# Optimization experiments

Hardware: AMD Instinct MI355X
Metric: run time of the kernel (lower is better)

Reference implementation:

```python
import jax, jax.numpy as jnp
import numpy as np

N = 100000   # nodes
E = 1600000  # edges
D = 128      # input feature dim
H = 128      # hidden dim
L = 3        # gnn layers
G = 64       # graphs in batch
C = 2        # classes


def setup_inputs() -> dict:
    key = jax.random.key(0)
    ks = jax.random.split(key, 12)
    s = 0.05
    x = jax.random.normal(ks[0], (N, D), jnp.float32)
    edge_index = jax.random.randint(ks[1], (2, E), 0, N, dtype=jnp.int32)
    batch = jnp.sort(jax.random.randint(ks[2], (N,), 0, G, dtype=jnp.int32))
    return {
        "x": x,
        "edge_index": edge_index,
        "batch": batch,
        "W0": jax.random.normal(ks[3], (D, H), jnp.float32) * s,
        "b0": jnp.zeros((H,), jnp.float32),
        "Wg": jax.random.normal(ks[4], (L, H, H), jnp.float32) * s,
        "bg": jnp.zeros((L, H), jnp.float32),
        "Wc1": jax.random.normal(ks[5], (H, H), jnp.float32) * s,
        "bc1": jnp.zeros((H,), jnp.float32),
        "Wc2": jax.random.normal(ks[6], (H, C), jnp.float32) * s,
        "bc2": jnp.zeros((C,), jnp.float32),
    }


def reference(x, edge_index, batch, W0, b0, Wg, bg, Wc1, bc1, Wc2, bc2):
    # --- GCN normalization with self-loops (PyG gcn_norm) ---
    src, dst = edge_index[0], edge_index[1]
    loops = jnp.arange(N, dtype=src.dtype)
    src_f = jnp.concatenate([src, loops])  # [E+N] message sources (x_j)
    dst_f = jnp.concatenate([dst, loops])  # [E+N] aggregation targets
    deg = jax.ops.segment_sum(jnp.ones((E + N,), x.dtype), dst_f, num_segments=N)
    dinv = jnp.where(deg > 0, jax.lax.rsqrt(deg), 0.0)
    norm = (dinv[src_f] * dinv[dst_f])[:, None]  # [E+N, 1]

    # --- input linear + relu (dropout is identity in eval mode) ---
    h = jax.nn.relu(x @ W0 + b0)  # [N, H]

    # --- stacked GCNConv layers with residual + relu ---
    for l in range(L):
        xw = h @ Wg[l]  # [N, H]
        agg = jax.ops.segment_sum(xw[src_f] * norm, dst_f, num_segments=N) + bg[l]
        h = jax.nn.relu(h + agg)

    # --- global add pool over graphs ---
    pooled = jax.ops.segment_sum(h, batch, num_segments=G)  # [G, H]

    # --- classifier MLP + softmax ---
    z = jax.nn.relu(pooled @ Wc1 + bc1)
    return jax.nn.softmax(z @ Wc2 + bc2, axis=-1)  # [G, C]
```

## Files before the change

### kernel.cpp

```cpp
#include <hip/hip_runtime.h>

#define NN 100000
#define NE 1600000
#define HD 128
#define NG 64
#define NL 3
#define NBK 391
#define NEB 391
#define CAP 4608
#define NRB 6250
#define FP4_SCALE 8.0f
#define FP4_INV   0.125f

typedef __attribute__((ext_vector_type(8))) short bf16x8;
typedef __attribute__((ext_vector_type(4))) float f32x4;
typedef __attribute__((ext_vector_type(2))) float f32x2;
union U4 { uint4 u; bf16x8 b; };


__device__ __forceinline__ unsigned f2bf(float f) {
    unsigned u = __float_as_uint(f);
    return (u + 0x7FFFu + ((u >> 16) & 1u)) >> 16;
}
__device__ __forceinline__ float bf_lo(unsigned w) { return __uint_as_float(w << 16); }
__device__ __forceinline__ float bf_hi(unsigned w) { return __uint_as_float(w & 0xFFFF0000u); }
__device__ __forceinline__ unsigned cvt_pk_bf16(float lo, float hi) {
    unsigned r;
    asm("v_cvt_pk_bf16_f32 %0, %1, %2" : "=v"(r) : "v"(lo), "v"(hi));
    return r;
}


__global__ __launch_bounds__(256) void k_pre(const float* __restrict__ W0,
                                             const float* __restrict__ Wg,
                                             unsigned* __restrict__ Wb,
                                             const int* __restrict__ src,
                                             const int* __restrict__ dst,
                                             int* __restrict__ gcur,
                                             unsigned* __restrict__ pairs,
                                             const int* __restrict__ batch,
                                             int* __restrict__ start) {
    int blk = blockIdx.x;
    if (blk < 32) {
        int gid = blk * 256 + threadIdx.x;
        for (int i = gid; i < 4 * 8192; i += 32 * 256) {
            int m = i >> 13;
            int r = i & 8191;
            int col = r & 127;
            int p = r >> 7;
            int k0, k1;
            if (m == 0) { k0 = 2 * p; k1 = 2 * p + 1; }
            else        { k0 = p;     k1 = p + 64;    }
            const float* Ws = (m == 0) ? W0 : (Wg + (m - 1) * 16384);
            float w0 = Ws[k0 * 128 + col];
            float w1 = Ws[k1 * 128 + col];
            Wb[m * 8192 + col * 64 + (((2 * p) ^ ((col & 7) << 3)) >> 1)] = (f2bf(w1) << 16) | f2bf(w0);
        }
    } else if (blk < 32 + NEB) {
        __shared__ int cnt[NBK];
        __shared__ int bse[NBK];
        __shared__ int rnk[NBK];
        for (int i = threadIdx.x; i < NBK; i += 256) { cnt[i] = 0; rnk[i] = 0; }
        __syncthreads();
        int base = (blk - 32) * 4096;
        int d[16];
#pragma unroll
        for (int j = 0; j < 16; j++) {
            int e = base + j * 256 + threadIdx.x;
            d[j] = (e < NE) ? dst[e] : -1;
            if (d[j] >= 0) atomicAdd(&cnt[((unsigned)d[j]) >> 8], 1);
        }
        __syncthreads();
        for (int i = threadIdx.x; i < NBK; i += 256) {
            int c = cnt[i];
            bse[i] = c ? atomicAdd(&gcur[i], c) : 0;
        }
        __syncthreads();
#pragma unroll
        for (int j = 0; j < 16; j++) {
            int e = base + j * 256 + threadIdx.x;
            if (e < NE) {
                int b = ((unsigned)d[j]) >> 8;
                int r = atomicAdd(&rnk[b], 1);
                int pos = bse[b] + r;
                if (pos < CAP)
                    pairs[(size_t)b * CAP + pos] = (unsigned)src[e] | (((unsigned)d[j] & 255u) << 17);
            }
        }
    } else {
        int i = (blk - 32 - NEB) * 256 + threadIdx.x;
        if (i >= NN) return;
        int b = batch[i];
        int prev = (i == 0) ? -1 : batch[i - 1];
        for (int g = prev + 1; g <= b; g++) start[g] = i;
        if (i == NN - 1) {
            for (int g = b + 1; g <= NG; g++) start[g] = NN;
        }
    }
}


__global__ __launch_bounds__(256) void k_bfill(const unsigned* __restrict__ pairs,
                                               const int* __restrict__ gcur,
                                               int* __restrict__ row_ptr, int* __restrict__ degA,
                                               float* __restrict__ dinv, unsigned* __restrict__ csr) {
    __shared__ int cnt[256];
    __shared__ int cur[256];
    __shared__ int wsum[4];
    int t = threadIdx.x, k = blockIdx.x;
    int base = k * CAP;
    int ne = min(gcur[k], CAP);
    cnt[t] = 0;
    __syncthreads();
    for (int e = t; e < ne; e += 256) atomicAdd(&cnt[pairs[base + e] >> 17], 1);
    __syncthreads();
    int v = cnt[t];
    int lane = t & 63, wv = t >> 6;
    int sc = v;
#pragma unroll
    for (int off = 1; off < 64; off <<= 1) {
        int n = __shfl_up(sc, off);
        if (lane >= off) sc += n;
    }
    if (lane == 63) wsum[wv] = sc;
    __syncthreads();
    int wbase = 0;
#pragma unroll
    for (int wi = 0; wi < 3; wi++) if (wi < wv) wbase += wsum[wi];
    int excl = base + wbase + sc - v;
    int node = (k << 8) + t;
    if (node < NN) {
        row_ptr[node] = excl;
        degA[node] = v;
        dinv[node] = rsqrtf((float)(v + 1));
    }
    cur[t] = excl;
    __syncthreads();
    for (int e = t; e < ne; e += 256) {
        unsigned p = pairs[base + e];
        int pos = atomicAdd(&cur[p >> 17], 1);
        csr[pos] = (p & 0x1FFFFu) << 6;
    }
}


template <int MODE>
__global__ __launch_bounds__(256) void k_mgemm(
    const float* __restrict__ Xf, const unsigned* __restrict__ Xb,
    const unsigned* __restrict__ Wb, const float* __restrict__ bias,
    const float* __restrict__ dinv, unsigned* __restrict__ Out) {
    __shared__ unsigned short Bt[128 * 128];
    {
        const uint4* s4 = (const uint4*)Wb;
        uint4* d4 = (uint4*)Bt;
        for (int i = threadIdx.x; i < 2048; i += 256) d4[i] = s4[i];
    }
    __syncthreads();

    int lane = threadIdx.x & 63;
    int l15 = lane & 15, q = lane >> 4;
    int rb = blockIdx.x * 4 + (threadIdx.x >> 6);
    if (rb >= NRB) return;
    int r0 = rb * 16;

    U4 a[4];
    if (MODE == 0) {
        const float* xrow = Xf + (size_t)(r0 + l15) * 128 + q * 8;
#pragma unroll
        for (int kk = 0; kk < 4; kk++) {
            float4 f0 = *(const float4*)(xrow + kk * 32);
            float4 f1 = *(const float4*)(xrow + kk * 32 + 4);
            a[kk].u.x = (f2bf(f0.y) << 16) | f2bf(f0.x);
            a[kk].u.y = (f2bf(f0.w) << 16) | f2bf(f0.z);
            a[kk].u.z = (f2bf(f1.y) << 16) | f2bf(f1.x);
            a[kk].u.w = (f2bf(f1.w) << 16) | f2bf(f1.z);
        }
    } else {
        const unsigned* xrow = Xb + (size_t)(r0 + l15) * 64 + q * 4;
#pragma unroll
        for (int kk = 0; kk < 4; kk++) a[kk].u = *(const uint4*)(xrow + kk * 16);
    }

    f32x4 acc[8];
#pragma unroll
    for (int ct = 0; ct < 8; ct++) acc[ct] = (f32x4){0.f, 0.f, 0.f, 0.f};
#pragma unroll
    for (int kk = 0; kk < 4; kk++) {
#pragma unroll
        for (int ct = 0; ct < 8; ct++) {
            int col = ct * 16 + l15;
            int off = col * 128 + ((kk * 32 + q * 8) ^ ((col & 7) << 3));
            U4 b;
            b.u = *(const uint4*)&Bt[off];
            acc[ct] = __builtin_amdgcn_mfma_f32_16x16x32_bf16(a[kk].b, b.b, acc[ct], 0, 0, 0);
        }
    }

    if (MODE == 0) {
        float bv[8];
#pragma unroll
        for (int ct = 0; ct < 8; ct++) bv[ct] = bias[ct * 16 + l15];
#pragma unroll
        for (int r = 0; r < 4; r++) {
            int row = r0 + q * 4 + r;
#pragma unroll
            for (int ct = 0; ct < 4; ct++) {
                float lo = fmaxf(acc[ct][r] + bv[ct], 0.f);
                float hi = fmaxf(acc[ct + 4][r] + bv[ct + 4], 0.f);
                Out[(size_t)row * 64 + ct * 16 + l15] = cvt_pk_bf16(lo, hi);
            }
        }
    } else {
#pragma unroll
        for (int r = 0; r < 4; r++) {
            int row = r0 + q * 4 + r;
            float sc = dinv[row] * FP4_SCALE;
            unsigned dw = __builtin_amdgcn_cvt_scalef32_pk_fp4_f32(0u, acc[0][r] * sc, acc[4][r] * sc, 1.0f, 0);
            dw = __builtin_amdgcn_cvt_scalef32_pk_fp4_f32(dw, acc[2][r] * sc, acc[6][r] * sc, 1.0f, 1);
            dw = __builtin_amdgcn_cvt_scalef32_pk_fp4_f32(dw, acc[1][r] * sc, acc[5][r] * sc, 1.0f, 2);
            dw = __builtin_amdgcn_cvt_scalef32_pk_fp4_f32(dw, acc[3][r] * sc, acc[7][r] * sc, 1.0f, 3);
            Out[(size_t)row * 16 + l15] = dw;
        }
    }
}


__global__ __launch_bounds__(256) void k_aggregate(const unsigned char* __restrict__ xb,
                                                   unsigned* __restrict__ hb,
                                                   const int* __restrict__ row_ptr,
                                                   const int* __restrict__ degA,
                                                   const unsigned* __restrict__ csr,
                                                   const float* __restrict__ dinv,
                                                   const float* __restrict__ bg) {
    int wave = threadIdx.x >> 6;
    int lane = threadIdx.x & 63;
    int q = lane >> 4;
    int l16 = lane & 15;
    int sub = l16 >> 3;
    int l8 = l16 & 7;
    int node = blockIdx.x * 16 + wave * 4 + q;
    unsigned e = (unsigned)row_ptr[node];
    unsigned e1 = e + (unsigned)degA[node];
    unsigned loff = (unsigned)l8 * 8u;

    f32x2 p0 = {0.f, 0.f}, p1 = {0.f, 0.f}, p2 = {0.f, 0.f}, p3 = {0.f, 0.f};
    f32x2 q0 = {0.f, 0.f}, q1 = {0.f, 0.f}, q2 = {0.f, 0.f}, q3 = {0.f, 0.f};

#define ACC8(V) \
    p0 += __builtin_amdgcn_cvt_scalef32_pk_f32_fp4((V).x, 1.0f, 0); \
    p1 += __builtin_amdgcn_cvt_scalef32_pk_f32_fp4((V).x, 1.0f, 1); \
    p2 += __builtin_amdgcn_cvt_scalef32_pk_f32_fp4((V).x, 1.0f, 2); \
    p3 += __builtin_amdgcn_cvt_scalef32_pk_f32_fp4((V).x, 1.0f, 3); \
    q0 += __builtin_amdgcn_cvt_scalef32_pk_f32_fp4((V).y, 1.0f, 0); \
    q1 += __builtin_amdgcn_cvt_scalef32_pk_f32_fp4((V).y, 1.0f, 1); \
    q2 += __builtin_amdgcn_cvt_scalef32_pk_f32_fp4((V).y, 1.0f, 2); \
    q3 += __builtin_amdgcn_cvt_scalef32_pk_f32_fp4((V).y, 1.0f, 3);

    for (; e + 7 < e1; e += 8) {
        unsigned o0 = csr[e + sub];
        unsigned o1 = csr[e + 2 + sub];
        unsigned o2 = csr[e + 4 + sub];
        unsigned o3 = csr[e + 6 + sub];
        uint2 v0 = *(const uint2*)(xb + (o0 + loff));
        uint2 v1 = *(const uint2*)(xb + (o1 + loff));
        uint2 v2 = *(const uint2*)(xb + (o2 + loff));
        uint2 v3 = *(const uint2*)(xb + (o3 + loff));
        ACC8(v0); ACC8(v1); ACC8(v2); ACC8(v3);
    }
    if (e + 3 < e1) {
        unsigned o0 = csr[e + sub];
        unsigned o1 = csr[e + 2 + sub];
        uint2 v0 = *(const uint2*)(xb + (o0 + loff));
        uint2 v1 = *(const uint2*)(xb + (o1 + loff));
        ACC8(v0); ACC8(v1);
        e += 4;
    }
    if (e + 1 < e1) {
        unsigned o = csr[e + sub];
        uint2 v = *(const uint2*)(xb + (o + loff));
        ACC8(v);
        e += 2;
    }
    if (e + (unsigned)sub < e1) {
        unsigned o = csr[e + sub];
        uint2 v = *(const uint2*)(xb + (o + loff));
        ACC8(v);
    }
#undef ACC8

    f32x2 s0 = sub ? q0 : p0;
    f32x2 s1 = sub ? q1 : p1;
    f32x2 s2 = sub ? q2 : p2;
    f32x2 s3 = sub ? q3 : p3;
    f32x2 t0 = sub ? p0 : q0;
    f32x2 t1 = sub ? p1 : q1;
    f32x2 t2 = sub ? p2 : q2;
    f32x2 t3 = sub ? p3 : q3;
    s0.x += __shfl_xor(t0.x, 8); s0.y += __shfl_xor(t0.y, 8);
    s1.x += __shfl_xor(t1.x, 8); s1.y += __shfl_xor(t1.y, 8);
    s2.x += __shfl_xor(t2.x, 8); s2.y += __shfl_xor(t2.y, 8);
    s3.x += __shfl_xor(t3.x, 8); s3.y += __shfl_xor(t3.y, 8);

    int j_e = 2 * l8 + sub;

    unsigned ovd = *(const unsigned*)(xb + (((unsigned)node << 6) + (unsigned)j_e * 4u));
    s0 += __builtin_amdgcn_cvt_scalef32_pk_f32_fp4(ovd, 1.0f, 0);
    s1 += __builtin_amdgcn_cvt_scalef32_pk_f32_fp4(ovd, 1.0f, 1);
    s2 += __builtin_amdgcn_cvt_scalef32_pk_f32_fp4(ovd, 1.0f, 2);
    s3 += __builtin_amdgcn_cvt_scalef32_pk_f32_fp4(ovd, 1.0f, 3);

    float di2 = dinv[node] * FP4_INV;
    float a[8] = {s0.x, s0.y, s1.x, s1.y, s2.x, s2.y, s3.x, s3.y};
    size_t hbase = (size_t)node * 64;
    unsigned hv0 = hb[hbase + j_e];
    unsigned hv1 = hb[hbase + j_e + 32];
    unsigned hv2 = hb[hbase + j_e + 16];
    unsigned hv3 = hb[hbase + j_e + 48];
    float hh[8] = {bf_lo(hv0), bf_hi(hv0), bf_lo(hv1), bf_hi(hv1),
                   bf_lo(hv2), bf_hi(hv2), bf_lo(hv3), bf_hi(hv3)};
    float gg[8] = {bg[j_e], bg[j_e + 64], bg[j_e + 32], bg[j_e + 96],
                   bg[j_e + 16], bg[j_e + 80], bg[j_e + 48], bg[j_e + 112]};
    float r[8];
#pragma unroll
    for (int i = 0; i < 8; i++) r[i] = fmaxf(hh[i] + di2 * a[i] + gg[i], 0.f);
    hb[hbase + j_e]      = cvt_pk_bf16(r[0], r[1]);
    hb[hbase + j_e + 32] = cvt_pk_bf16(r[2], r[3]);
    hb[hbase + j_e + 16] = cvt_pk_bf16(r[4], r[5]);
    hb[hbase + j_e + 48] = cvt_pk_bf16(r[6], r[7]);
}


__global__ __launch_bounds__(128) void k_pool(const unsigned* __restrict__ hb,
                                              const int* __restrict__ start,
                                              float* __restrict__ pooled) {
    int g = blockIdx.x >> 4;
    int c = blockIdx.x & 15;
    int s = start[g], e = start[g + 1];
    int len = e - s;
    if (len <= 0) return;
    int chunk = (len + 15) >> 4;
    int r0 = s + c * chunk;
    int r1 = min(e, r0 + chunk);
    if (r0 >= r1) return;
    int jj = threadIdx.x & 63;
    int half = threadIdx.x >> 6;
    float ax = 0.f, ay = 0.f;
    for (int r = r0 + half; r < r1; r += 2) {
        unsigned v = hb[(size_t)r * 64 + jj];
        ax += bf_lo(v);
        ay += bf_hi(v);
    }
    atomicAdd(&pooled[g * 128 + jj], ax);
    atomicAdd(&pooled[g * 128 + jj + 64], ay);
}


__global__ __launch_bounds__(128) void k_classify(const float* __restrict__ pooled,
                                                  const float* __restrict__ Wc1,
                                                  const float* __restrict__ bc1,
                                                  const float* __restrict__ Wc2,
                                                  const float* __restrict__ bc2,
                                                  float* __restrict__ out) {
    __shared__ float p[128];
    __shared__ float r0s[128];
    __shared__ float r1s[128];
    int g = blockIdx.x;
    int j = threadIdx.x;
    p[j] = pooled[g * 128 + j];
    __syncthreads();
    float acc = bc1[j];
#pragma unroll 4
    for (int k = 0; k < 128; k++) acc = fmaf(p[k], Wc1[k * 128 + j], acc);
    float z = fmaxf(acc, 0.f);
    r0s[j] = z * Wc2[j * 2 + 0];
    r1s[j] = z * Wc2[j * 2 + 1];
    __syncthreads();
    for (int st = 64; st > 0; st >>= 1) {
        if (j < st) { r0s[j] += r0s[j + st]; r1s[j] += r1s[j + st]; }
        __syncthreads();
    }
    if (j == 0) {
        float l0 = r0s[0] + bc2[0];
        float l1 = r1s[0] + bc2[1];
        float m = fmaxf(l0, l1);
        float e0 = expf(l0 - m), e1 = expf(l1 - m);
        float inv = 1.f / (e0 + e1);
        out[g * 2 + 0] = e0 * inv;
        out[g * 2 + 1] = e1 * inv;
    }
}


extern "C" void kernel_launch(void* const* d_in, const int* in_sizes, int n_in,
                              void* d_out, int out_size, void* d_ws, size_t ws_size,
                              hipStream_t stream) {
    (void)in_sizes; (void)n_in; (void)out_size;

    const float* x     = (const float*)d_in[0];
    const int*   ei    = (const int*)d_in[1];
    const int*   batch = (const int*)d_in[2];
    const float* W0    = (const float*)d_in[3];
    const float* b0    = (const float*)d_in[4];
    const float* Wg    = (const float*)d_in[5];
    const float* bg    = (const float*)d_in[6];
    const float* Wc1   = (const float*)d_in[7];
    const float* bc1   = (const float*)d_in[8];
    const float* Wc2   = (const float*)d_in[9];
    const float* bc2   = (const float*)d_in[10];
    float* out = (float*)d_out;

    const int* srcp = ei;
    const int* dstp = ei + NE;

    char* w = (char*)d_ws;
    auto alloc = [&](size_t bytes) {
        char* p = w;
        w += (bytes + 255) & ~(size_t)255;
        return p;
    };
    int*      gcur    = (int*)alloc((size_t)NBK * 4);
    float*    pooled  = (float*)alloc((size_t)NG * HD * 4);
    size_t zbytes = (size_t)((char*)w - (char*)gcur);
    unsigned* hb      = (unsigned*)alloc((size_t)NN * 64 * 4);
    unsigned* xws4    = (unsigned*)alloc((size_t)NN * 16 * 4);
    float*    dinv    = (float*)alloc((size_t)NN * 4);
    int*      row_ptr = (int*)alloc((size_t)NN * 4);
    int*      degA    = (int*)alloc((size_t)NN * 4);
    unsigned* csr     = (unsigned*)alloc((size_t)NBK * CAP * 4);
    unsigned* pairs   = (unsigned*)alloc((size_t)NBK * CAP * 4);
    unsigned* Wb      = (unsigned*)alloc((size_t)4 * 8192 * 4);
    int*      start   = (int*)alloc((NG + 1) * 4);
    if ((size_t)(w - (char*)d_ws) > ws_size) return;

    hipMemsetAsync(gcur, 0, zbytes, stream);

    k_pre<<<32 + NEB + 391, 256, 0, stream>>>(W0, Wg, Wb, srcp, dstp, gcur, pairs, batch, start);
    k_bfill<<<NBK, 256, 0, stream>>>(pairs, gcur, row_ptr, degA, dinv, csr);

    int gb = (NRB + 3) / 4;
    k_mgemm<0><<<gb, 256, 0, stream>>>(x, nullptr, Wb, b0, nullptr, hb);
    for (int l = 0; l < NL; l++) {
        k_mgemm<1><<<gb, 256, 0, stream>>>(nullptr, hb, Wb + (size_t)(l + 1) * 8192, nullptr, dinv, xws4);
        k_aggregate<<<NRB, 256, 0, stream>>>((const unsigned char*)xws4, hb, row_ptr, degA, csr, dinv, bg + l * HD);
    }
    k_pool<<<NG * 16, 128, 0, stream>>>(hb, start, pooled);
    k_classify<<<NG, 128, 0, stream>>>(pooled, Wc1, bc1, Wc2, bc2, out);
}
```

Baseline: 221.4 us.

## Sort nodes by degree for aggregation and use nontemporal CSR/h accesses

Adds a degree histogram in k_bfill and a new k_perm kernel that counting-sorts nodes into descending-degree order. k_aggregate then processes nodes through this permutation, so the 16 nodes sharing a wave group have similar edge counts and lanes diverge less in the edge loop. CSR index and hidden-state loads and stores are also marked nontemporal so the streaming data does not crowd the gathered features out of cache. The cost is an extra kernel launch, global atomics, and scattered row access to hb and row_ptr in aggregation.

```diff
diff --git a/kernel.cpp b/kernel.cpp
--- a/kernel.cpp
+++ b/kernel.cpp
@@ -103,7 +103,8 @@
 __global__ __launch_bounds__(256) void k_bfill(const unsigned* __restrict__ pairs,
                                                const int* __restrict__ gcur,
                                                int* __restrict__ row_ptr, int* __restrict__ degA,
-                                               float* __restrict__ dinv, unsigned* __restrict__ csr) {
+                                               float* __restrict__ dinv, unsigned* __restrict__ csr,
+                                               int* __restrict__ dbins) {
     __shared__ int cnt[256];
     __shared__ int cur[256];
     __shared__ int wsum[4];
@@ -133,6 +134,7 @@
         row_ptr[node] = excl;
         degA[node] = v;
         dinv[node] = rsqrtf((float)(v + 1));
+        atomicAdd(&dbins[v > 63 ? 63 : v], 1);
     }
     cur[t] = excl;
     __syncthreads();
@@ -141,6 +143,27 @@
         int pos = atomicAdd(&cur[p >> 17], 1);
         csr[pos] = (p & 0x1FFFFu) << 6;
     }
+}
+
+
+__global__ __launch_bounds__(256) void k_perm(const int* __restrict__ degA,
+                                              const int* __restrict__ dbins,
+                                              int* __restrict__ cursor,
+                                              int* __restrict__ perm) {
+    __shared__ int base[64];
+    int t = threadIdx.x;
+    if (t < 64) {
+        int b = 0;
+        for (int d = 63; d > t; d--) b += dbins[d];
+        base[t] = b;
+    }
+    __syncthreads();
+    int node = blockIdx.x * 256 + t;
+    if (node >= NN) return;
+    int d = degA[node];
+    if (d > 63) d = 63;
+    int pos = base[d] + atomicAdd(&cursor[d], 1);
+    perm[pos] = node;
 }
 
 
@@ -231,14 +254,15 @@
                                                    const int* __restrict__ degA,
                                                    const unsigned* __restrict__ csr,
                                                    const float* __restrict__ dinv,
-                                                   const float* __restrict__ bg) {
+                                                   const float* __restrict__ bg,
+                                                   const int* __restrict__ perm) {
     int wave = threadIdx.x >> 6;
     int lane = threadIdx.x & 63;
     int q = lane >> 4;
     int l16 = lane & 15;
     int sub = l16 >> 3;
     int l8 = l16 & 7;
-    int node = blockIdx.x * 16 + wave * 4 + q;
+    int node = perm[blockIdx.x * 16 + wave * 4 + q];
     unsigned e = (unsigned)row_ptr[node];
     unsigned e1 = e + (unsigned)degA[node];
     unsigned loff = (unsigned)l8 * 8u;
@@ -257,10 +281,10 @@
     q3 += __builtin_amdgcn_cvt_scalef32_pk_f32_fp4((V).y, 1.0f, 3);
 
     for (; e + 7 < e1; e += 8) {
-        unsigned o0 = csr[e + sub];
-        unsigned o1 = csr[e + 2 + sub];
-        unsigned o2 = csr[e + 4 + sub];
-        unsigned o3 = csr[e + 6 + sub];
+        unsigned o0 = __builtin_nontemporal_load(&csr[e + sub]);
+        unsigned o1 = __builtin_nontemporal_load(&csr[e + 2 + sub]);
+        unsigned o2 = __builtin_nontemporal_load(&csr[e + 4 + sub]);
+        unsigned o3 = __builtin_nontemporal_load(&csr[e + 6 + sub]);
         uint2 v0 = *(const uint2*)(xb + (o0 + loff));
         uint2 v1 = *(const uint2*)(xb + (o1 + loff));
         uint2 v2 = *(const uint2*)(xb + (o2 + loff));
@@ -268,21 +292,21 @@
         ACC8(v0); ACC8(v1); ACC8(v2); ACC8(v3);
     }
     if (e + 3 < e1) {
-        unsigned o0 = csr[e + sub];
-        unsigned o1 = csr[e + 2 + sub];
+        unsigned o0 = __builtin_nontemporal_load(&csr[e + sub]);
+        unsigned o1 = __builtin_nontemporal_load(&csr[e + 2 + sub]);
         uint2 v0 = *(const uint2*)(xb + (o0 + loff));
         uint2 v1 = *(const uint2*)(xb + (o1 + loff));
         ACC8(v0); ACC8(v1);
         e += 4;
     }
     if (e + 1 < e1) {
-        unsigned o = csr[e + sub];
+        unsigned o = __builtin_nontemporal_load(&csr[e + sub]);
         uint2 v = *(const uint2*)(xb + (o + loff));
         ACC8(v);
         e += 2;
     }
     if (e + (unsigned)sub < e1) {
-        unsigned o = csr[e + sub];
+        unsigned o = __builtin_nontemporal_load(&csr[e + sub]);
         uint2 v = *(const uint2*)(xb + (o + loff));
         ACC8(v);
     }
@@ -312,10 +336,10 @@
     float di2 = dinv[node] * FP4_INV;
     float a[8] = {s0.x, s0.y, s1.x, s1.y, s2.x, s2.y, s3.x, s3.y};
     size_t hbase = (size_t)node * 64;
-    unsigned hv0 = hb[hbase + j_e];
-    unsigned hv1 = hb[hbase + j_e + 32];
-    unsigned hv2 = hb[hbase + j_e + 16];
-    unsigned hv3 = hb[hbase + j_e + 48];
+    unsigned hv0 = __builtin_nontemporal_load(&hb[hbase + j_e]);
+    unsigned hv1 = __builtin_nontemporal_load(&hb[hbase + j_e + 32]);
+    unsigned hv2 = __builtin_nontemporal_load(&hb[hbase + j_e + 16]);
+    unsigned hv3 = __builtin_nontemporal_load(&hb[hbase + j_e + 48]);
     float hh[8] = {bf_lo(hv0), bf_hi(hv0), bf_lo(hv1), bf_hi(hv1),
                    bf_lo(hv2), bf_hi(hv2), bf_lo(hv3), bf_hi(hv3)};
     float gg[8] = {bg[j_e], bg[j_e + 64], bg[j_e + 32], bg[j_e + 96],
@@ -323,10 +347,10 @@
     float r[8];
 #pragma unroll
     for (int i = 0; i < 8; i++) r[i] = fmaxf(hh[i] + di2 * a[i] + gg[i], 0.f);
-    hb[hbase + j_e]      = cvt_pk_bf16(r[0], r[1]);
-    hb[hbase + j_e + 32] = cvt_pk_bf16(r[2], r[3]);
-    hb[hbase + j_e + 16] = cvt_pk_bf16(r[4], r[5]);
-    hb[hbase + j_e + 48] = cvt_pk_bf16(r[6], r[7]);
+    __builtin_nontemporal_store(cvt_pk_bf16(r[0], r[1]), &hb[hbase + j_e]);
+    __builtin_nontemporal_store(cvt_pk_bf16(r[2], r[3]), &hb[hbase + j_e + 32]);
+    __builtin_nontemporal_store(cvt_pk_bf16(r[4], r[5]), &hb[hbase + j_e + 16]);
+    __builtin_nontemporal_store(cvt_pk_bf16(r[6], r[7]), &hb[hbase + j_e + 48]);
 }
 
 
@@ -420,12 +444,15 @@
     };
     int*      gcur    = (int*)alloc((size_t)NBK * 4);
     float*    pooled  = (float*)alloc((size_t)NG * HD * 4);
+    int*      dbins   = (int*)alloc(64 * 4);
+    int*      cursor  = (int*)alloc(64 * 4);
     size_t zbytes = (size_t)((char*)w - (char*)gcur);
     unsigned* hb      = (unsigned*)alloc((size_t)NN * 64 * 4);
     unsigned* xws4    = (unsigned*)alloc((size_t)NN * 16 * 4);
     float*    dinv    = (float*)alloc((size_t)NN * 4);
     int*      row_ptr = (int*)alloc((size_t)NN * 4);
     int*      degA    = (int*)alloc((size_t)NN * 4);
+    int*      perm    = (int*)alloc((size_t)NN * 4);
     unsigned* csr     = (unsigned*)alloc((size_t)NBK * CAP * 4);
     unsigned* pairs   = (unsigned*)alloc((size_t)NBK * CAP * 4);
     unsigned* Wb      = (unsigned*)alloc((size_t)4 * 8192 * 4);
@@ -435,13 +462,14 @@
     hipMemsetAsync(gcur, 0, zbytes, stream);
 
     k_pre<<<32 + NEB + 391, 256, 0, stream>>>(W0, Wg, Wb, srcp, dstp, gcur, pairs, batch, start);
-    k_bfill<<<NBK, 256, 0, stream>>>(pairs, gcur, row_ptr, degA, dinv, csr);
+    k_bfill<<<NBK, 256, 0, stream>>>(pairs, gcur, row_ptr, degA, dinv, csr, dbins);
+    k_perm<<<NBK, 256, 0, stream>>>(degA, dbins, cursor, perm);
 
     int gb = (NRB + 3) / 4;
     k_mgemm<0><<<gb, 256, 0, stream>>>(x, nullptr, Wb, b0, nullptr, hb);
     for (int l = 0; l < NL; l++) {
         k_mgemm<1><<<gb, 256, 0, stream>>>(nullptr, hb, Wb + (size_t)(l + 1) * 8192, nullptr, dinv, xws4);
-        k_aggregate<<<NRB, 256, 0, stream>>>((const unsigned char*)xws4, hb, row_ptr, degA, csr, dinv, bg + l * HD);
+        k_aggregate<<<NRB, 256, 0, stream>>>((const unsigned char*)xws4, hb, row_ptr, degA, csr, dinv, bg + l * HD, perm);
     }
     k_pool<<<NG * 16, 128, 0, stream>>>(hb, start, pooled);
     k_classify<<<NG, 128, 0, stream>>>(pooled, Wc1, bc1, Wc2, bc2, out);
```

Measured after the change: 780.1 us. 3.52x slower.
